# Kernel optimization log

Measured on AMD Instinct MI355X. Metric: run time of the kernel, lower is better.

## Reference

```python
import jax, jax.numpy as jnp
import numpy as np

T, B, L = 1024, 128, 128


def setup_inputs() -> dict:
    key = jax.random.key(0)
    k1, k2, k3, k4, k5 = jax.random.split(key, 5)
    return {
        "predictions": jax.random.normal(k1, (T, B, L), dtype=jnp.float32),
        "targets": jax.random.randint(k2, (T, B), 0, L, dtype=jnp.int64),
        "mask": jnp.ones((T, B), dtype=jnp.int32),
        "transitions": jax.random.normal(k3, (L, L), dtype=jnp.float32),
        "start_scores": jax.random.normal(k4, (L,), dtype=jnp.float32),
        "end_scores": jax.random.normal(k5, (L,), dtype=jnp.float32),
    }


def _numerator(predictions, targets, maskf, transitions, start_scores, end_scores):
    batch_idx = jnp.arange(predictions.shape[1])
    # emission score of the gold tag at every step: [T, B]
    emit = jnp.take_along_axis(predictions, targets[:, :, None], axis=2)[..., 0]
    trans = transitions[targets[:-1], targets[1:]]  # [T-1, B]
    score = start_scores[targets[0]] + emit[0]
    score = score + jnp.sum((trans + emit[1:]) * maskf[1:], axis=0)
    last_idx = jnp.sum(maskf, axis=0).astype(jnp.int32) - 1
    score = score + end_scores[targets[last_idx, batch_idx]]
    return score  # [B]


def _denominator(predictions, maskb, transitions, start_scores, end_scores):
    score0 = start_scores + predictions[0]  # [B, L]

    def step(score, inp):
        pred_i, mask_i = inp  # [B, L], [B]
        # [B, L, L]: prev-label axis 1, next-label axis 2
        s = score[:, :, None] + transitions[None, :, :] + pred_i[:, None, :]
        new_score = jax.scipy.special.logsumexp(s, axis=1)
        score = jnp.where(mask_i[:, None], new_score, score)
        return score, None

    score, _ = jax.lax.scan(step, score0, (predictions[1:], maskb[1:]))
    score = score + end_scores
    return jax.scipy.special.logsumexp(score, axis=1)  # [B]


def reference(predictions, targets, mask, transitions, start_scores, end_scores):
    maskf = mask.astype(predictions.dtype)
    maskb = mask.astype(bool)
    num = _numerator(predictions, targets, maskf, transitions, start_scores, end_scores)
    den = _denominator(predictions, maskb, transitions, start_scores, end_scores)
    return jnp.mean(den - num)
```

## Files before the change

kernel.cpp:

```cpp
#include <hip/hip_runtime.h>

#define T_DIM 1024
#define B_DIM 128
#define L_DIM 128

__device__ __forceinline__ float readlane0_f32(float v) {
    return __uint_as_float(__builtin_amdgcn_readfirstlane(__float_as_uint(v)));
}

__global__ __launch_bounds__(256, 1)
void crf_den_kernel(const float* __restrict__ pred,
                    const int*   __restrict__ mask,
                    const float* __restrict__ trans,
                    const float* __restrict__ start_s,
                    const float* __restrict__ end_s,
                    float* __restrict__ den_out)
{
    const int b     = blockIdx.x;
    const int tid   = threadIdx.x;
    const int w     = tid >> 6;
    const int lane  = tid & 63;
    const int sub   = lane & 31;
    const int kh    = lane >> 5;
    const int state = w * 32 + sub;
    const int kbase = kh * 64;

    float etr[64];
#pragma unroll
    for (int ii = 0; ii < 64; ++ii)
        etr[ii] = __expf(trans[(kbase + ii) * L_DIM + state]);

    __shared__ __align__(16) float es_lds[2][L_DIM];
    __shared__ __align__(16) float c_lds[2][4];

    float score = start_s[state] + pred[b * L_DIM + state];

    float p_next = pred[(1 * B_DIM + b) * L_DIM + state];
    int   m_next = mask[1 * B_DIM + b];

    for (int t = 1; t < T_DIM; ++t) {
        const float p_cur = p_next;
        const int   mk    = m_next;
        if (t + 1 < T_DIM) {
            p_next = pred[((t + 1) * B_DIM + b) * L_DIM + state];
            m_next = mask[(t + 1) * B_DIM + b];
        }
        const int buf = t & 1;

        const float c_w = readlane0_f32(score);
        const float es  = __expf(score - c_w);
        if (lane < 32) es_lds[buf][state] = es;
        if (lane == 0) c_lds[buf][w] = c_w;
        __syncthreads();

        const float* esb = &es_lds[buf][kbase];
        float a0 = 0.f, a1 = 0.f, a2 = 0.f, a3 = 0.f;
#pragma unroll
        for (int ii = 0; ii < 32; ii += 4) {
            const float4 e4 = *(const float4*)&esb[ii];
            a0 = fmaf(e4.x, etr[ii + 0], a0);
            a1 = fmaf(e4.y, etr[ii + 1], a1);
            a0 = fmaf(e4.z, etr[ii + 2], a0);
            a1 = fmaf(e4.w, etr[ii + 3], a1);
        }
#pragma unroll
        for (int ii = 32; ii < 64; ii += 4) {
            const float4 e4 = *(const float4*)&esb[ii];
            a2 = fmaf(e4.x, etr[ii + 0], a2);
            a3 = fmaf(e4.y, etr[ii + 1], a3);
            a2 = fmaf(e4.z, etr[ii + 2], a2);
            a3 = fmaf(e4.w, etr[ii + 3], a3);
        }

        const float4 cv = *(const float4*)&c_lds[buf][0];
        const float c   = fmaxf(fmaxf(cv.x, cv.y), fmaxf(cv.z, cv.w));
        const float cA  = (kh == 0) ? cv.x : cv.z;
        const float cB  = (kh == 0) ? cv.y : cv.w;
        const float fA  = __expf(cA - c);
        const float fB  = __expf(cB - c);

        const float part = fA * (a0 + a1) + fB * (a2 + a3);
        const float acc  = part + __shfl_xor(part, 32, 64);

        const float ns = c + __logf(acc) + p_cur;
        if (mk) score = ns;
    }

    const float v = score + end_s[state];
    float wm = v;
#pragma unroll
    for (int off = 32; off >= 1; off >>= 1)
        wm = fmaxf(wm, __shfl_xor(wm, off, 64));
    float e = __expf(v - wm);
#pragma unroll
    for (int off = 32; off >= 1; off >>= 1)
        e += __shfl_xor(e, off, 64);
    if (lane == 0) { c_lds[0][w] = wm; c_lds[1][w] = e; }
    __syncthreads();
    if (tid == 0) {
        const float m0 = fmaxf(fmaxf(c_lds[0][0], c_lds[0][1]),
                               fmaxf(c_lds[0][2], c_lds[0][3]));
        float s = 0.f;
#pragma unroll
        for (int ww = 0; ww < 4; ++ww)
            s += c_lds[1][ww] * __expf(c_lds[0][ww] - m0);
        den_out[b] = m0 + __logf(s * 0.5f);
    }
}

__global__ __launch_bounds__(256, 1)
void crf_num_kernel(const float* __restrict__ pred,
                    const int*   __restrict__ targets,
                    const int*   __restrict__ mask,
                    const float* __restrict__ trans,
                    const float* __restrict__ start_s,
                    const float* __restrict__ end_s,
                    float* __restrict__ num_out)
{
    const int b = blockIdx.x;
    const int k = threadIdx.x;

    float local = 0.f;
    int   msum  = 0;
    for (int t = k; t < T_DIM; t += 256) {
        const int mk = mask[t * B_DIM + b];
        msum += mk;
        if (t >= 1) {
            const int tp = targets[(t - 1) * B_DIM + b];
            const int tc = targets[t * B_DIM + b];
            const float c = trans[tp * L_DIM + tc] +
                            pred[(t * B_DIM + b) * L_DIM + tc];
            local += c * (float)mk;
        }
    }

#pragma unroll
    for (int off = 32; off >= 1; off >>= 1) {
        local += __shfl_xor(local, off, 64);
        msum  += __shfl_xor(msum,  off, 64);
    }
    __shared__ float sred[4];
    __shared__ int   ired[4];
    const int w = k >> 6;
    if ((k & 63) == 0) { sred[w] = local; ired[w] = msum; }
    __syncthreads();
    if (k == 0) {
        float tot = sred[0] + sred[1] + sred[2] + sred[3];
        const int ms = ired[0] + ired[1] + ired[2] + ired[3];
        const int t0 = targets[b];
        tot += start_s[t0] + pred[b * L_DIM + t0];
        const int last = ms - 1;
        tot += end_s[targets[last * B_DIM + b]];
        num_out[b] = tot;
    }
}

__global__ __launch_bounds__(128, 1)
void crf_reduce_kernel(const float* __restrict__ den,
                       const float* __restrict__ num,
                       float* __restrict__ out)
{
    const int j = threadIdx.x;
    float d = den[j] - num[j];
#pragma unroll
    for (int off = 32; off >= 1; off >>= 1)
        d += __shfl_xor(d, off, 64);
    __shared__ float s[2];
    if ((j & 63) == 0) s[j >> 6] = d;
    __syncthreads();
    if (j == 0) out[0] = (s[0] + s[1]) * (1.0f / (float)B_DIM);
}

extern "C" void kernel_launch(void* const* d_in, const int* in_sizes, int n_in,
                              void* d_out, int out_size, void* d_ws, size_t ws_size,
                              hipStream_t stream)
{
    const float* pred    = (const float*)d_in[0];
    const int*   targets = (const int*)  d_in[1];
    const int*   mask    = (const int*)  d_in[2];
    const float* trans   = (const float*)d_in[3];
    const float* start_s = (const float*)d_in[4];
    const float* end_s   = (const float*)d_in[5];
    float* out = (float*)d_out;

    float* den = (float*)d_ws;
    float* num = den + B_DIM;

    crf_den_kernel<<<B_DIM, 256, 0, stream>>>(pred, mask, trans, start_s, end_s, den);
    crf_num_kernel<<<B_DIM, 256, 0, stream>>>(pred, targets, mask, trans, start_s, end_s, num);
    crf_reduce_kernel<<<1, 128, 0, stream>>>(den, num, out);
}
```

Measured before the change: 782.6 us.

## Carry CRF forward scores in scaled linear domain with integer exponent tracking

The denominator recursion now keeps scores in the linear (exp) domain. Each step rescales by a power of two taken from one lane's exponent bits and accumulates the integer exponent, replacing the per-step exp/log with ldexp and a multiply by a prefetched exp(pred). Blocks grow to 512 threads so each thread covers 32 of the reduction terms instead of 64. This shortens the serial chain per step. It adds a cross-quarter shuffle reduction, replicated LDS writes, and a hand-placed barrier. Underflow or overflow is possible if states within a wave differ by a large dynamic range.

```diff
diff --git a/kernel.cpp b/kernel.cpp
--- a/kernel.cpp
+++ b/kernel.cpp
@@ -1,4 +1,5 @@
 #include <hip/hip_runtime.h>
+#include <math.h>
 
 #define T_DIM 1024
 #define B_DIM 128
@@ -8,7 +9,7 @@
     return __uint_as_float(__builtin_amdgcn_readfirstlane(__float_as_uint(v)));
 }
 
-__global__ __launch_bounds__(256, 1)
+__global__ __launch_bounds__(512, 1)
 void crf_den_kernel(const float* __restrict__ pred,
                     const int*   __restrict__ mask,
                     const float* __restrict__ trans,
@@ -20,91 +21,103 @@
     const int tid   = threadIdx.x;
     const int w     = tid >> 6;
     const int lane  = tid & 63;
-    const int sub   = lane & 31;
-    const int kh    = lane >> 5;
-    const int state = w * 32 + sub;
-    const int kbase = kh * 64;
-
-    float etr[64];
-#pragma unroll
-    for (int ii = 0; ii < 64; ++ii)
+    const int sub   = lane & 15;
+    const int kq    = lane >> 4;
+    const int state = w * 16 + sub;
+    const int kbase = kq * 32;
+
+    float etr[32];
+#pragma unroll
+    for (int ii = 0; ii < 32; ++ii)
         etr[ii] = __expf(trans[(kbase + ii) * L_DIM + state]);
 
-    __shared__ __align__(16) float es_lds[2][L_DIM];
-    __shared__ __align__(16) float c_lds[2][4];
-
-    float score = start_s[state] + pred[b * L_DIM + state];
-
-    float p_next = pred[(1 * B_DIM + b) * L_DIM + state];
-    int   m_next = mask[1 * B_DIM + b];
+    __shared__ __align__(16) float es_lds[2][4 * 132];
+    __shared__ __align__(16) int   e_lds[2][8];
+    __shared__ float fsum_lds[8];
+
+    float u = __expf(start_s[state] + pred[b * L_DIM + state]);
+    int   D = 0;
+
+    float ep_next = __expf(pred[(1 * B_DIM + b) * L_DIM + state]);
+    float p2      = pred[(2 * B_DIM + b) * L_DIM + state];
+    int   mk_next = mask[1 * B_DIM + b];
+    int   mk2     = mask[2 * B_DIM + b];
 
     for (int t = 1; t < T_DIM; ++t) {
-        const float p_cur = p_next;
-        const int   mk    = m_next;
-        if (t + 1 < T_DIM) {
-            p_next = pred[((t + 1) * B_DIM + b) * L_DIM + state];
-            m_next = mask[(t + 1) * B_DIM + b];
-        }
+        const float ep_cur = ep_next;
+        const int   mk     = mk_next;
+        const int tpre = (t + 2 < T_DIM) ? (t + 2) : (T_DIM - 1);
+        const float p3  = pred[(tpre * B_DIM + b) * L_DIM + state];
+        const int   mk3 = mask[tpre * B_DIM + b];
+        ep_next = __expf(p2);
+        p2 = p3; mk_next = mk2; mk2 = mk3;
+
         const int buf = t & 1;
 
-        const float c_w = readlane0_f32(score);
-        const float es  = __expf(score - c_w);
-        if (lane < 32) es_lds[buf][state] = es;
-        if (lane == 0) c_lds[buf][w] = c_w;
-        __syncthreads();
-
-        const float* esb = &es_lds[buf][kbase];
-        float a0 = 0.f, a1 = 0.f, a2 = 0.f, a3 = 0.f;
-#pragma unroll
-        for (int ii = 0; ii < 32; ii += 4) {
-            const float4 e4 = *(const float4*)&esb[ii];
-            a0 = fmaf(e4.x, etr[ii + 0], a0);
-            a1 = fmaf(e4.y, etr[ii + 1], a1);
-            a0 = fmaf(e4.z, etr[ii + 2], a0);
-            a1 = fmaf(e4.w, etr[ii + 3], a1);
-        }
-#pragma unroll
-        for (int ii = 32; ii < 64; ii += 4) {
-            const float4 e4 = *(const float4*)&esb[ii];
-            a2 = fmaf(e4.x, etr[ii + 0], a2);
-            a3 = fmaf(e4.y, etr[ii + 1], a3);
-            a2 = fmaf(e4.z, etr[ii + 2], a2);
-            a3 = fmaf(e4.w, etr[ii + 3], a3);
-        }
-
-        const float4 cv = *(const float4*)&c_lds[buf][0];
-        const float c   = fmaxf(fmaxf(cv.x, cv.y), fmaxf(cv.z, cv.w));
-        const float cA  = (kh == 0) ? cv.x : cv.z;
-        const float cB  = (kh == 0) ? cv.y : cv.w;
-        const float fA  = __expf(cA - c);
-        const float fB  = __expf(cB - c);
-
-        const float part = fA * (a0 + a1) + fB * (a2 + a3);
-        const float acc  = part + __shfl_xor(part, 32, 64);
-
-        const float ns = c + __logf(acc) + p_cur;
-        if (mk) score = ns;
-    }
-
-    const float v = score + end_s[state];
-    float wm = v;
+        const unsigned ub      = __float_as_uint(readlane0_f32(u));
+        const int      Ebiased = (int)(ub >> 23);
+        const float    scale   = __uint_as_float((unsigned)(254 - Ebiased) << 23);
+        const float    us      = u * scale;
+        if (lane < 16) {
+            float* dst = &es_lds[buf][state];
+#pragma unroll
+            for (int c = 0; c < 4; ++c) dst[c * 132] = us;
+        }
+        if (lane == 0) e_lds[buf][w] = Ebiased;
+
+        asm volatile("s_waitcnt lgkmcnt(0)" ::: "memory");
+        __builtin_amdgcn_s_barrier();
+        __builtin_amdgcn_sched_barrier(0);
+
+        const float* esb = &es_lds[buf][kq * 132 + kbase];
+        const int4  eL = *(const int4*)&e_lds[buf][0];
+        const int4  eH = *(const int4*)&e_lds[buf][4];
+
+        float accA = 0.f, accB = 0.f;
+#pragma unroll
+        for (int c = 0; c < 4; ++c) {
+            const float4 e4 = *(const float4*)&esb[c * 4];
+            accA = fmaf(e4.x, etr[c * 4 + 0], accA);
+            accA = fmaf(e4.y, etr[c * 4 + 1], accA);
+            accA = fmaf(e4.z, etr[c * 4 + 2], accA);
+            accA = fmaf(e4.w, etr[c * 4 + 3], accA);
+        }
+#pragma unroll
+        for (int c = 4; c < 8; ++c) {
+            const float4 e4 = *(const float4*)&esb[c * 4];
+            accB = fmaf(e4.x, etr[c * 4 + 0], accB);
+            accB = fmaf(e4.y, etr[c * 4 + 1], accB);
+            accB = fmaf(e4.z, etr[c * 4 + 2], accB);
+            accB = fmaf(e4.w, etr[c * 4 + 3], accB);
+        }
+
+        const int emax = max(max(max(eL.x, eL.y), max(eL.z, eL.w)),
+                             max(max(eH.x, eH.y), max(eH.z, eH.w)));
+        int eA, eB;
+        switch (kq) {
+            case 0: eA = eL.x; eB = eL.y; break;
+            case 1: eA = eL.z; eB = eL.w; break;
+            case 2: eA = eH.x; eB = eH.y; break;
+            default: eA = eH.z; eB = eH.w; break;
+        }
+        float part = ldexpf(accA, eA - emax) + ldexpf(accB, eB - emax);
+        part += __shfl_xor(part, 16, 64);
+        part += __shfl_xor(part, 32, 64);
+
+        if (mk) { u = part * ep_cur; D += (emax - 127); }
+    }
+
+    float val = (kq == 0) ? u * __expf(end_s[state]) : 0.f;
 #pragma unroll
     for (int off = 32; off >= 1; off >>= 1)
-        wm = fmaxf(wm, __shfl_xor(wm, off, 64));
-    float e = __expf(v - wm);
-#pragma unroll
-    for (int off = 32; off >= 1; off >>= 1)
-        e += __shfl_xor(e, off, 64);
-    if (lane == 0) { c_lds[0][w] = wm; c_lds[1][w] = e; }
+        val += __shfl_xor(val, off, 64);
+    if (lane == 0) fsum_lds[w] = val;
     __syncthreads();
     if (tid == 0) {
-        const float m0 = fmaxf(fmaxf(c_lds[0][0], c_lds[0][1]),
-                               fmaxf(c_lds[0][2], c_lds[0][3]));
-        float s = 0.f;
-#pragma unroll
-        for (int ww = 0; ww < 4; ++ww)
-            s += c_lds[1][ww] * __expf(c_lds[0][ww] - m0);
-        den_out[b] = m0 + __logf(s * 0.5f);
+        float tot = 0.f;
+#pragma unroll
+        for (int ww = 0; ww < 8; ++ww) tot += fsum_lds[ww];
+        den_out[b] = logf(tot) + (float)D * 0.69314718055994531f;
     }
 }
 
@@ -186,7 +199,7 @@
     float* den = (float*)d_ws;
     float* num = den + B_DIM;
 
-    crf_den_kernel<<<B_DIM, 256, 0, stream>>>(pred, mask, trans, start_s, end_s, den);
+    crf_den_kernel<<<B_DIM, 512, 0, stream>>>(pred, mask, trans, start_s, end_s, den);
     crf_num_kernel<<<B_DIM, 256, 0, stream>>>(pred, targets, mask, trans, start_s, end_s, num);
     crf_reduce_kernel<<<1, 128, 0, stream>>>(den, num, out);
 }
```

New measurement: 735.7 us. -6.0%, faster.
